# Kernel optimization log

Measured on AMD Instinct MI355X. Metric: run time of the kernel, lower is better.

The kernel has to match this reference:

```python
import jax, jax.numpy as jnp
import numpy as np

B, CQ, CKV, LQ, LKV, HEADS = 4, 1024, 1024, 2048, 2048, 16


def _conv1x1(W, x):
    # Conv1d with kernel size 1: out[b,o,l] = sum_i W[o,i] * x[b,i,l]
    return jnp.einsum('oi,bil->bol', W, x)


def _linear_interp(x, L_out):
    # F.interpolate(mode='linear', align_corners=False) on (B,C,L)
    B_, C_, L_in = x.shape
    if L_in == L_out:
        return x
    scale = L_in / L_out
    pos = (jnp.arange(L_out, dtype=x.dtype) + 0.5) * scale - 0.5
    pos = jnp.clip(pos, 0.0, L_in - 1)
    lo = jnp.floor(pos).astype(jnp.int32)
    hi = jnp.minimum(lo + 1, L_in - 1)
    w = (pos - lo.astype(x.dtype))
    return x[:, :, lo] * (1.0 - w) + x[:, :, hi] * w


def setup_inputs() -> dict:
    key = jax.random.key(0)
    ks = jax.random.split(key, 7)
    winit = 1.0 / np.sqrt(CQ)
    return {
        'query': jax.random.normal(ks[0], (B, CQ, LQ), dtype=jnp.float32),
        'context': jax.random.normal(ks[1], (B, CKV, LKV), dtype=jnp.float32),
        'Wq': jax.random.normal(ks[2], (CQ, CQ), dtype=jnp.float32) * winit,
        'Wk': jax.random.normal(ks[3], (CQ, CKV), dtype=jnp.float32) * winit,
        'Wv': jax.random.normal(ks[4], (CQ, CKV), dtype=jnp.float32) * winit,
        'Wo': jax.random.normal(ks[5], (CQ, CQ), dtype=jnp.float32) * winit,
        'bo': jnp.zeros((CQ,), dtype=jnp.float32),
        'heads': HEADS,
    }


def reference(query, context, Wq, Wk, Wv, Wo, bo, heads):
    B_, Cq, Lq = query.shape
    H = heads
    D = Cq // H
    scale = D ** (-0.5)
    q = _conv1x1(Wq, query).reshape(B_, H, D, Lq)
    k = _conv1x1(Wk, context)
    v = _conv1x1(Wv, context)
    if k.shape[2] != Lq:
        k = _linear_interp(k, Lq)
        v = _linear_interp(v, Lq)
    k = k.reshape(B_, H, D, Lq)
    v = v.reshape(B_, H, D, Lq)
    attn = jnp.einsum('bhdi,bhdj->bhij', q, k) * scale
    attn = jax.nn.softmax(attn, axis=-1)
    out = jnp.einsum('bhij,bhdj->bhdi', attn, v).reshape(B_, Cq, Lq)
    return _conv1x1(Wo, out) + bo[None, :, None] + query
```

## Files before the change

### kernel.cpp

```cpp
#include <hip/hip_runtime.h>
#include <hip/hip_bf16.h>

typedef __bf16 bf16;
typedef __attribute__((ext_vector_type(8))) __bf16 bf16x8;
typedef __attribute__((ext_vector_type(4))) __bf16 bf16x4;
typedef __attribute__((ext_vector_type(4))) float f32x4;
typedef __attribute__((ext_vector_type(8))) float f32x8;
typedef __attribute__((ext_vector_type(16))) float f32x16;
typedef unsigned int uint2v __attribute__((ext_vector_type(2)));

#define B_ 4
#define C_ 1024
#define L_ 2048
#define H_ 16
#define D_ 64

__device__ __forceinline__ int swz(int row, int g) {
    return row * 64 + (((g ^ row) & 7) << 3);
}

__device__ __forceinline__ void async_ld16(const bf16* g, bf16* l) {
    __builtin_amdgcn_global_load_lds(
        (const __attribute__((address_space(1))) unsigned int*)g,
        (__attribute__((address_space(3))) unsigned int*)l, 16, 0, 0);
}

__device__ __forceinline__ float fast_exp2(float x) {
    float r;
    asm("v_exp_f32 %0, %1" : "=v"(r) : "v"(x));
    return r;
}

__global__ void cvt_w4(const float* __restrict__ wq, const float* __restrict__ wk,
                       const float* __restrict__ wv, const float* __restrict__ wo,
                       bf16* __restrict__ oq, bf16* __restrict__ ok,
                       bf16* __restrict__ ov, bf16* __restrict__ oo,
                       float qscale) {
    int z = blockIdx.y;
    const float* in = (z == 0) ? wq : (z == 1) ? wk : (z == 2) ? wv : wo;
    bf16* out       = (z == 0) ? oq : (z == 1) ? ok : (z == 2) ? ov : oo;
    float scale     = (z == 0) ? qscale : 1.0f;
    int i = (blockIdx.x * blockDim.x + threadIdx.x) * 4;
    f32x4 x = *(const f32x4*)&in[i];
    bf16x4 y;
#pragma unroll
    for (int e = 0; e < 4; e++) y[e] = (bf16)(x[e] * scale);
    *(bf16x4*)&out[i] = y;
}

__global__ void transpose_cvt(const float* __restrict__ in, bf16* __restrict__ out) {
    __shared__ bf16 s[32][33];
    int z  = blockIdx.z;
    int c0 = blockIdx.x * 32;
    int r0 = blockIdx.y * 32;
    const float* pin = in + (size_t)z * C_ * L_;
    bf16* pout       = out + (size_t)z * L_ * C_;
#pragma unroll
    for (int k = 0; k < 4; k++) {
        int r = r0 + threadIdx.y + k * 8;
        s[threadIdx.y + k * 8][threadIdx.x] = (bf16)pin[(size_t)r * L_ + c0 + threadIdx.x];
    }
    __syncthreads();
#pragma unroll
    for (int k = 0; k < 4; k++) {
        int c = c0 + threadIdx.y + k * 8;
        pout[(size_t)c * C_ + r0 + threadIdx.x] = s[threadIdx.x][threadIdx.y + k * 8];
    }
}

__global__ __launch_bounds__(256) void gemm_tn(const bf16* __restrict__ A,
                                               const bf16* __restrict__ Wt,
                                               bf16* __restrict__ Dd,
                                               int M, int N, int K) {
    __shared__ __align__(16) bf16 As[2][128 * 64];
    __shared__ __align__(16) bf16 Ws[2][128 * 64];
    int m0 = blockIdx.x * 128, n0 = blockIdx.y * 128;
    int t = threadIdx.x;
    int lane = t & 63, wave = t >> 6;
    int l15 = lane & 15, quad = lane >> 4;
    int wm = (wave >> 1) * 64, wn = (wave & 1) * 64;

    f32x4 acc[4][4];
#pragma unroll
    for (int i = 0; i < 4; i++)
#pragma unroll
        for (int j = 0; j < 4; j++) {
            f32x4 z = {0.f, 0.f, 0.f, 0.f};
            acc[i][j] = z;
        }

    int r8 = lane >> 3;
    int gl = (((lane & 7) ^ r8) & 7) * 8;
    const bf16* aG = A  + (size_t)(m0 + wave * 32 + r8) * K + gl;
    const bf16* wG = Wt + (size_t)(n0 + wave * 32 + r8) * K + gl;

    auto STAGE = [&](int buf, int kk) {
#pragma unroll
        for (int p = 0; p < 4; p++) {
            async_ld16(aG + kk + (size_t)p * 8 * K, &As[buf][(wave * 32 + p * 8) * 64]);
            async_ld16(wG + kk + (size_t)p * 8 * K, &Ws[buf][(wave * 32 + p * 8) * 64]);
        }
    };

    STAGE(0, 0);
    int KT = K >> 6;
    for (int it = 0; it < KT; ++it) {
        int cur = it & 1;
        if (it + 1 < KT) {
            STAGE(cur ^ 1, (it + 1) << 6);
            asm volatile("s_waitcnt vmcnt(8)" ::: "memory");
        } else {
            asm volatile("s_waitcnt vmcnt(0)" ::: "memory");
        }
        __builtin_amdgcn_s_barrier();
        asm volatile("" ::: "memory");
#pragma unroll
        for (int ks = 0; ks < 2; ks++) {
            bf16x8 af[4], bfr[4];
#pragma unroll
            for (int i = 0; i < 4; i++)
                af[i] = *(const bf16x8*)&As[cur][swz(wm + i * 16 + l15, ks * 4 + quad)];
#pragma unroll
            for (int i = 0; i < 4; i++)
                bfr[i] = *(const bf16x8*)&Ws[cur][swz(wn + i * 16 + l15, ks * 4 + quad)];
#pragma unroll
            for (int mt = 0; mt < 4; mt++)
#pragma unroll
                for (int nt = 0; nt < 4; nt++)
                    acc[mt][nt] = __builtin_amdgcn_mfma_f32_16x16x32_bf16(
                        af[mt], bfr[nt], acc[mt][nt], 0, 0, 0);
        }
        asm volatile("" ::: "memory");
        __builtin_amdgcn_s_barrier();
    }
#pragma unroll
    for (int mt = 0; mt < 4; mt++)
#pragma unroll
        for (int nt = 0; nt < 4; nt++)
#pragma unroll
            for (int r = 0; r < 4; r++) {
                int row = m0 + wm + mt * 16 + quad * 4 + r;
                int col = n0 + wn + nt * 16 + l15;
                Dd[(size_t)row * N + col] = (bf16)acc[mt][nt][r];
            }
}

__global__ __launch_bounds__(256) void gemm_v_tn(const bf16* __restrict__ Wv,
                                                 const bf16* __restrict__ ctxT_,
                                                 bf16* __restrict__ vv_) {
    __shared__ __align__(16) bf16 As[2][128 * 64];
    __shared__ __align__(16) bf16 Ws[2][128 * 64];
    int zb = blockIdx.z;
    const bf16* Bz = ctxT_ + (size_t)zb * L_ * C_;
    bf16* vv       = vv_   + (size_t)zb * C_ * L_;

    int m0 = blockIdx.x * 128, n0 = blockIdx.y * 128;
    int t = threadIdx.x;
    int lane = t & 63, wave = t >> 6;
    int l15 = lane & 15, quad = lane >> 4;
    int wm = (wave >> 1) * 64, wn = (wave & 1) * 64;

    f32x4 acc[4][4];
#pragma unroll
    for (int i = 0; i < 4; i++)
#pragma unroll
        for (int j = 0; j < 4; j++) {
            f32x4 z = {0.f, 0.f, 0.f, 0.f};
            acc[i][j] = z;
        }

    int r8 = lane >> 3;
    int gl = (((lane & 7) ^ r8) & 7) * 8;
    const bf16* aG = Wv + (size_t)(m0 + wave * 32 + r8) * C_ + gl;
    const bf16* wG = Bz + (size_t)(n0 + wave * 32 + r8) * C_ + gl;

    auto STAGE = [&](int buf, int kk) {
#pragma unroll
        for (int p = 0; p < 4; p++) {
            async_ld16(aG + kk + (size_t)p * 8 * C_, &As[buf][(wave * 32 + p * 8) * 64]);
            async_ld16(wG + kk + (size_t)p * 8 * C_, &Ws[buf][(wave * 32 + p * 8) * 64]);
        }
    };

    STAGE(0, 0);
    const int KT = C_ >> 6;
    for (int it = 0; it < KT; ++it) {
        int cur = it & 1;
        if (it + 1 < KT) {
            STAGE(cur ^ 1, (it + 1) << 6);
            asm volatile("s_waitcnt vmcnt(8)" ::: "memory");
        } else {
            asm volatile("s_waitcnt vmcnt(0)" ::: "memory");
        }
        __builtin_amdgcn_s_barrier();
        asm volatile("" ::: "memory");
#pragma unroll
        for (int ks = 0; ks < 2; ks++) {
            bf16x8 af[4], bfr[4];
#pragma unroll
            for (int i = 0; i < 4; i++)
                af[i] = *(const bf16x8*)&As[cur][swz(wm + i * 16 + l15, ks * 4 + quad)];
#pragma unroll
            for (int i = 0; i < 4; i++)
                bfr[i] = *(const bf16x8*)&Ws[cur][swz(wn + i * 16 + l15, ks * 4 + quad)];
#pragma unroll
            for (int mt = 0; mt < 4; mt++)
#pragma unroll
                for (int nt = 0; nt < 4; nt++)
                    acc[mt][nt] = __builtin_amdgcn_mfma_f32_16x16x32_bf16(
                        af[mt], bfr[nt], acc[mt][nt], 0, 0, 0);
        }
        asm volatile("" ::: "memory");
        __builtin_amdgcn_s_barrier();
    }
#pragma unroll
    for (int mt = 0; mt < 4; mt++)
#pragma unroll
        for (int nt = 0; nt < 4; nt++)
#pragma unroll
            for (int r = 0; r < 4; r++) {
                int row = m0 + wm + mt * 16 + quad * 4 + r;
                int col = n0 + wn + nt * 16 + l15;
                vv[(size_t)row * L_ + col] = (bf16)acc[mt][nt][r];
            }
}

__global__ __launch_bounds__(256) void gemm_o_final(const bf16* __restrict__ A_,
                                                    const bf16* __restrict__ Wt,
                                                    const float* __restrict__ query_,
                                                    const float* __restrict__ bo,
                                                    float* __restrict__ out_) {
    __shared__ __align__(16) bf16 smem[4 * 128 * 64];

    int zb = blockIdx.z;
    const bf16* A      = A_     + (size_t)zb * L_ * C_;
    const float* query = query_ + (size_t)zb * C_ * L_;
    float* out         = out_   + (size_t)zb * C_ * L_;

    int l0 = blockIdx.x * 128, n0 = blockIdx.y * 128;
    int t = threadIdx.x;
    int lane = t & 63, wave = t >> 6;
    int l15 = lane & 15, quad = lane >> 4;
    int wm = (wave >> 1) * 64, wn = (wave & 1) * 64;

    f32x4 acc[4][4];
#pragma unroll
    for (int i = 0; i < 4; i++)
#pragma unroll
        for (int j = 0; j < 4; j++) {
            f32x4 z = {0.f, 0.f, 0.f, 0.f};
            acc[i][j] = z;
        }

    int r8 = lane >> 3;
    int gl = (((lane & 7) ^ r8) & 7) * 8;
    const bf16* aG = A  + (size_t)(l0 + wave * 32 + r8) * C_ + gl;
    const bf16* wG = Wt + (size_t)(n0 + wave * 32 + r8) * C_ + gl;

    auto STAGE = [&](int buf, int kk) {
        bf16* Ab = smem + buf * 8192;
        bf16* Wb = smem + 16384 + buf * 8192;
#pragma unroll
        for (int p = 0; p < 4; p++) {
            async_ld16(aG + kk + (size_t)p * 8 * C_, &Ab[(wave * 32 + p * 8) * 64]);
            async_ld16(wG + kk + (size_t)p * 8 * C_, &Wb[(wave * 32 + p * 8) * 64]);
        }
    };

    STAGE(0, 0);
    const int KT = C_ >> 6;
    for (int it = 0; it < KT; ++it) {
        int cur = it & 1;
        if (it + 1 < KT) {
            STAGE(cur ^ 1, (it + 1) << 6);
            asm volatile("s_waitcnt vmcnt(8)" ::: "memory");
        } else {
            asm volatile("s_waitcnt vmcnt(0)" ::: "memory");
        }
        __builtin_amdgcn_s_barrier();
        asm volatile("" ::: "memory");
        const bf16* Ab = smem + cur * 8192;
        const bf16* Wb = smem + 16384 + cur * 8192;
#pragma unroll
        for (int ks = 0; ks < 2; ks++) {
            bf16x8 af[4], bfr[4];
#pragma unroll
            for (int i = 0; i < 4; i++)
                af[i] = *(const bf16x8*)&Ab[swz(wm + i * 16 + l15, ks * 4 + quad)];
#pragma unroll
            for (int i = 0; i < 4; i++)
                bfr[i] = *(const bf16x8*)&Wb[swz(wn + i * 16 + l15, ks * 4 + quad)];
#pragma unroll
            for (int mt = 0; mt < 4; mt++)
#pragma unroll
                for (int nt = 0; nt < 4; nt++)
                    acc[mt][nt] = __builtin_amdgcn_mfma_f32_16x16x32_bf16(
                        af[mt], bfr[nt], acc[mt][nt], 0, 0, 0);
        }
        asm volatile("" ::: "memory");
        __builtin_amdgcn_s_barrier();
    }
    __syncthreads();

    bf16 (*Ts)[136] = (bf16 (*)[136])smem;
#pragma unroll
    for (int mt = 0; mt < 4; mt++)
#pragma unroll
        for (int nt = 0; nt < 4; nt++)
#pragma unroll
            for (int r = 0; r < 4; r++)
                Ts[wn + nt * 16 + l15][wm + mt * 16 + quad * 4 + r] = (bf16)acc[mt][nt][r];
    __syncthreads();
#pragma unroll
    for (int j = 0; j < 8; j++) {
        int idx = t + 256 * j;
        int cl  = idx >> 4;
        int ll8 = (idx & 15) * 8;
        int c   = n0 + cl;
        size_t goff = (size_t)c * L_ + l0 + ll8;
        bf16x8 y = *(const bf16x8*)&Ts[cl][ll8];
        f32x8 q = *(const f32x8*)&query[goff];
        float bias = bo[c];
        f32x8 o;
#pragma unroll
        for (int e = 0; e < 8; e++)
            o[e] = (float)y[e] + bias + q[e];
        *(f32x8*)&out[goff] = o;
    }
}

__global__ __launch_bounds__(256) void flash_attn(const bf16* qT,
                                                  const bf16* __restrict__ kT,
                                                  const bf16* __restrict__ v,
                                                  bf16* oT) {
    __shared__ __align__(16) bf16 Ks[2][64 * 64];
    __shared__ __align__(16) bf16 Vs[2][64 * 64];
    int i0 = blockIdx.x * 128;
    int h  = blockIdx.y;
    int zb = blockIdx.z;
    int t = threadIdx.x, lane = t & 63, wave = t >> 6;
    int l31 = lane & 31, kh = lane >> 5;

    const bf16* qB = qT + (size_t)zb * L_ * C_ + (size_t)h * D_;
    const bf16* kB = kT + (size_t)zb * L_ * C_ + (size_t)h * D_;
    const bf16* vB = v  + (size_t)zb * C_ * L_ + (size_t)h * D_ * L_;
    bf16* oB       = oT + (size_t)zb * L_ * C_ + (size_t)h * D_;

    bf16x8 qf[4];
#pragma unroll
    for (int kt = 0; kt < 4; kt++)
        qf[kt] = *(const bf16x8*)&qB[(size_t)(i0 + wave * 32 + l31) * C_ +
                                     kt * 16 + kh * 8];

    f32x16 acc_o[2];
#pragma unroll
    for (int dt = 0; dt < 2; dt++)
#pragma unroll
        for (int r = 0; r < 16; r++) acc_o[dt][r] = 0.f;
    f32x16 acc_l;
#pragma unroll
    for (int r = 0; r < 16; r++) acc_l[r] = 0.f;
    f32x16 z16;
#pragma unroll
    for (int r = 0; r < 16; r++) z16[r] = 0.f;

    bf16x8 onesf;
#pragma unroll
    for (int e = 0; e < 8; e++) onesf[e] = (bf16)1.0f;

    int r8 = lane >> 3;
    int gl = (((lane & 7) ^ r8) & 7) * 8;
    const bf16* kG = kB + (size_t)(wave * 16 + r8) * C_ + gl;
    const bf16* vG = vB + (size_t)(wave * 16 + r8) * L_ + gl;

    auto STAGE = [&](int buf, int j0n) {
#pragma unroll
        for (int p = 0; p < 2; p++) {
            async_ld16(kG + (size_t)j0n * C_ + (size_t)p * 8 * C_,
                       &Ks[buf][(wave * 16 + p * 8) * 64]);
            async_ld16(vG + j0n + (size_t)p * 8 * L_,
                       &Vs[buf][(wave * 16 + p * 8) * 64]);
        }
    };

    STAGE(0, 0);

    const int NT = L_ / 64;
    for (int it = 0; it < NT; ++it) {
        int cur = it & 1;
        if (it + 1 < NT) {
            STAGE(cur ^ 1, (it + 1) * 64);
            asm volatile("s_waitcnt vmcnt(4)" ::: "memory");
        } else {
            asm volatile("s_waitcnt vmcnt(0)" ::: "memory");
        }
        __builtin_amdgcn_s_barrier();
        asm volatile("" ::: "memory");

        const bf16* kb = &Ks[cur][0];
        const bf16* vb = &Vs[cur][0];

#pragma unroll
        for (int jt = 0; jt < 2; jt++) {
            f32x16 s;
            {
                bf16x8 a = *(const bf16x8*)&kb[swz(jt * 32 + l31, kh)];
                s = __builtin_amdgcn_mfma_f32_32x32x16_bf16(a, qf[0], z16, 0, 0, 0);
            }
#pragma unroll
            for (int kt = 1; kt < 4; kt++) {
                bf16x8 a = *(const bf16x8*)&kb[swz(jt * 32 + l31, kt * 2 + kh)];
                s = __builtin_amdgcn_mfma_f32_32x32x16_bf16(a, qf[kt], s, 0, 0, 0);
            }
            unsigned w[4][2];
#pragma unroll
            for (int q = 0; q < 4; q++)
#pragma unroll
                for (int c = 0; c < 2; c++) {
                    float p0 = fast_exp2(s[q * 4 + 2 * c]);
                    float p1 = fast_exp2(s[q * 4 + 2 * c + 1]);
                    asm("v_cvt_pk_bf16_f32 %0, %1, %2"
                        : "=v"(w[q][c]) : "v"(p0), "v"(p1));
                }
#pragma unroll
            for (int kp = 0; kp < 2; kp++) {
                int ks = jt * 2 + kp;
                uint2v r0 = __builtin_amdgcn_permlane32_swap(
                    w[kp * 2][0], w[kp * 2 + 1][0], false, false);
                uint2v r1 = __builtin_amdgcn_permlane32_swap(
                    w[kp * 2][1], w[kp * 2 + 1][1], false, false);
                union { unsigned u[4]; bf16x8 v8; } af;
                af.u[0] = r0[0]; af.u[1] = r1[0];
                af.u[2] = r0[1]; af.u[3] = r1[1];
#pragma unroll
                for (int dt = 0; dt < 2; dt++) {
                    bf16x8 b = *(const bf16x8*)&vb[swz(dt * 32 + l31, ks * 2 + kh)];
                    acc_o[dt] = __builtin_amdgcn_mfma_f32_32x32x16_bf16(
                        af.v8, b, acc_o[dt], 0, 0, 0);
                }
                acc_l = __builtin_amdgcn_mfma_f32_32x32x16_bf16(
                    af.v8, onesf, acc_l, 0, 0, 0);
            }
        }
        asm volatile("" ::: "memory");
        __builtin_amdgcn_s_barrier();
    }

    float inv[16];
#pragma unroll
    for (int r = 0; r < 16; r++) inv[r] = __builtin_amdgcn_rcpf(acc_l[r]);
#pragma unroll
    for (int dt = 0; dt < 2; dt++)
#pragma unroll
        for (int q = 0; q < 4; q++)
#pragma unroll
            for (int r = 0; r < 4; r++) {
                int row = i0 + wave * 32 + 8 * q + 4 * kh + r;
                oB[(size_t)row * C_ + dt * 32 + l31] =
                    (bf16)(acc_o[dt][q * 4 + r] * inv[q * 4 + r]);
            }
}

extern "C" void kernel_launch(void* const* d_in, const int* in_sizes, int n_in,
                              void* d_out, int out_size, void* d_ws, size_t ws_size,
                              hipStream_t stream) {
    const float* query   = (const float*)d_in[0];
    const float* context = (const float*)d_in[1];
    const float* Wq = (const float*)d_in[2];
    const float* Wk = (const float*)d_in[3];
    const float* Wv = (const float*)d_in[4];
    const float* Wo = (const float*)d_in[5];
    const float* bo = (const float*)d_in[6];
    float* out = (float*)d_out;

    const size_t Sw = (size_t)C_ * C_;
    size_t need_batched = (4 * Sw + 3 * (size_t)B_ * L_ * C_) * sizeof(bf16);
    int nb = (ws_size >= need_batched) ? B_ : 1;

    const size_t Sslot = (size_t)nb * L_ * C_;
    bf16* WqB = (bf16*)d_ws;
    bf16* WkB = WqB + Sw;
    bf16* WvB = WkB + Sw;
    bf16* WoB = WvB + Sw;
    bf16* slotA = WoB + Sw;
    bf16* slotB = slotA + Sslot;
    bf16* slotC = slotB + Sslot;

    cvt_w4<<<dim3((unsigned)(Sw / 4 / 256), 4), 256, 0, stream>>>(
        Wq, Wk, Wv, Wo, WqB, WkB, WvB, WoB, 0.1803368801111204f);

    dim3 tb(32, 8);
    dim3 tg(L_ / 32, C_ / 32, nb);
    dim3 gg(nb * L_ / 128, C_ / 128);
    dim3 vg(C_ / 128, L_ / 128, nb);
    dim3 zg(L_ / 128, C_ / 128, nb);
    dim3 fg(L_ / 128, H_, nb);

    for (int b0 = 0; b0 < B_; b0 += nb) {
        const float* qx = query   + (size_t)b0 * C_ * L_;
        const float* cx = context + (size_t)b0 * C_ * L_;
        float* ob       = out     + (size_t)b0 * C_ * L_;

        bf16* vscr = (bf16*)ob;

        transpose_cvt<<<tg, tb, 0, stream>>>(qx, slotA);
        gemm_tn<<<gg, 256, 0, stream>>>(slotA, WqB, slotB, nb * L_, C_, C_);
        transpose_cvt<<<tg, tb, 0, stream>>>(cx, slotA);
        gemm_tn<<<gg, 256, 0, stream>>>(slotA, WkB, slotC, nb * L_, C_, C_);
        gemm_v_tn<<<vg, 256, 0, stream>>>(WvB, slotA, vscr);
        flash_attn<<<fg, 256, 0, stream>>>(slotB, slotC, vscr, slotB);
        gemm_o_final<<<zg, 256, 0, stream>>>(slotB, WoB, qx, bo, ob);
    }
}
```

Measured before the change: 333.9 us.

## Fuse Q/K/V projections and transposes, swizzle block order, triple-buffer attention

Merges the two transpose kernels into one launch and the three projection GEMMs into one grid with a segment index, so fewer launches run and each grid is fuller. GEMM epilogues now stage through LDS for vectorized 16-byte stores. Block indices are remapped across groups of eight in the GEMM and attention grids, apparently to spread neighbouring tiles across XCDs for L2 locality. Flash attention moves to a three-stage K/V pipeline, which uses more LDS and may reduce occupancy. The context transpose is stored in the output buffer as scratch, which relies on that buffer being large enough.

Result: faster. 309.9 us (-7.2%).

```diff
diff --git a/kernel.cpp b/kernel.cpp
--- a/kernel.cpp
+++ b/kernel.cpp
@@ -48,13 +48,18 @@
     *(bf16x4*)&out[i] = y;
 }
 
-__global__ void transpose_cvt(const float* __restrict__ in, bf16* __restrict__ out) {
+__global__ void transpose_cvt2(const float* __restrict__ q,
+                               const float* __restrict__ c,
+                               bf16* __restrict__ qo, bf16* __restrict__ co,
+                               int nb) {
     __shared__ bf16 s[32][33];
     int z  = blockIdx.z;
+    const float* pin;
+    bf16* pout;
+    if (z < nb) { pin = q + (size_t)z * C_ * L_;        pout = qo + (size_t)z * L_ * C_; }
+    else        { pin = c + (size_t)(z - nb) * C_ * L_; pout = co + (size_t)(z - nb) * L_ * C_; }
     int c0 = blockIdx.x * 32;
     int r0 = blockIdx.y * 32;
-    const float* pin = in + (size_t)z * C_ * L_;
-    bf16* pout       = out + (size_t)z * L_ * C_;
 #pragma unroll
     for (int k = 0; k < 4; k++) {
         int r = r0 + threadIdx.y + k * 8;
@@ -63,18 +68,53 @@
     __syncthreads();
 #pragma unroll
     for (int k = 0; k < 4; k++) {
-        int c = c0 + threadIdx.y + k * 8;
-        pout[(size_t)c * C_ + r0 + threadIdx.x] = s[threadIdx.x][threadIdx.y + k * 8];
-    }
-}
-
-__global__ __launch_bounds__(256) void gemm_tn(const bf16* __restrict__ A,
-                                               const bf16* __restrict__ Wt,
-                                               bf16* __restrict__ Dd,
-                                               int M, int N, int K) {
-    __shared__ __align__(16) bf16 As[2][128 * 64];
-    __shared__ __align__(16) bf16 Ws[2][128 * 64];
-    int m0 = blockIdx.x * 128, n0 = blockIdx.y * 128;
+        int cc = c0 + threadIdx.y + k * 8;
+        pout[(size_t)cc * C_ + r0 + threadIdx.x] = s[threadIdx.x][threadIdx.y + k * 8];
+    }
+}
+
+__global__ __launch_bounds__(256) void gemm_fused3(const bf16* __restrict__ qT,
+                                                   const bf16* __restrict__ ctxT,
+                                                   const bf16* __restrict__ Wq,
+                                                   const bf16* __restrict__ Wk,
+                                                   const bf16* __restrict__ Wv,
+                                                   bf16* __restrict__ qP,
+                                                   bf16* __restrict__ kP,
+                                                   bf16* __restrict__ vP,
+                                                   int nb) {
+    __shared__ __align__(16) bf16 smem[4 * 128 * 64];
+
+    int seg = blockIdx.y;
+    int r   = blockIdx.x;
+    int cpx = nb << 4;
+    int lg  = (r & 7) * cpx + (r >> 3);
+
+    const bf16 *aP, *bP;
+    bf16* dP;
+    int S;
+    if (seg == 0) {
+        int m_idx = lg >> 3, n_idx = lg & 7;
+        aP = qT + (size_t)m_idx * 128 * C_;
+        bP = Wq + (size_t)n_idx * 128 * C_;
+        dP = qP + (size_t)m_idx * 128 * C_ + n_idx * 128;
+        S = C_;
+    } else if (seg == 1) {
+        int m_idx = lg >> 3, n_idx = lg & 7;
+        aP = ctxT + (size_t)m_idx * 128 * C_;
+        bP = Wk + (size_t)n_idx * 128 * C_;
+        dP = kP + (size_t)m_idx * 128 * C_ + n_idx * 128;
+        S = C_;
+    } else {
+        int m_idx = lg & 7;
+        int nt    = lg >> 3;
+        int zb    = nt >> 4;
+        int nc0   = (nt & 15) * 128;
+        aP = Wv + (size_t)m_idx * 128 * C_;
+        bP = ctxT + (size_t)nt * 128 * C_;
+        dP = vP + (size_t)zb * C_ * L_ + (size_t)m_idx * 128 * L_ + nc0;
+        S = L_;
+    }
+
     int t = threadIdx.x;
     int lane = t & 63, wave = t >> 6;
     int l15 = lane & 15, quad = lane >> 4;
@@ -91,94 +131,16 @@
 
     int r8 = lane >> 3;
     int gl = (((lane & 7) ^ r8) & 7) * 8;
-    const bf16* aG = A  + (size_t)(m0 + wave * 32 + r8) * K + gl;
-    const bf16* wG = Wt + (size_t)(n0 + wave * 32 + r8) * K + gl;
+    const bf16* aG = aP + (size_t)(wave * 32 + r8) * C_ + gl;
+    const bf16* wG = bP + (size_t)(wave * 32 + r8) * C_ + gl;
 
     auto STAGE = [&](int buf, int kk) {
+        bf16* Ab = smem + buf * 8192;
+        bf16* Wb = smem + 16384 + buf * 8192;
 #pragma unroll
         for (int p = 0; p < 4; p++) {
-            async_ld16(aG + kk + (size_t)p * 8 * K, &As[buf][(wave * 32 + p * 8) * 64]);
-            async_ld16(wG + kk + (size_t)p * 8 * K, &Ws[buf][(wave * 32 + p * 8) * 64]);
-        }
-    };
-
-    STAGE(0, 0);
-    int KT = K >> 6;
-    for (int it = 0; it < KT; ++it) {
-        int cur = it & 1;
-        if (it + 1 < KT) {
-            STAGE(cur ^ 1, (it + 1) << 6);
-            asm volatile("s_waitcnt vmcnt(8)" ::: "memory");
-        } else {
-            asm volatile("s_waitcnt vmcnt(0)" ::: "memory");
-        }
-        __builtin_amdgcn_s_barrier();
-        asm volatile("" ::: "memory");
-#pragma unroll
-        for (int ks = 0; ks < 2; ks++) {
-            bf16x8 af[4], bfr[4];
-#pragma unroll
-            for (int i = 0; i < 4; i++)
-                af[i] = *(const bf16x8*)&As[cur][swz(wm + i * 16 + l15, ks * 4 + quad)];
-#pragma unroll
-            for (int i = 0; i < 4; i++)
-                bfr[i] = *(const bf16x8*)&Ws[cur][swz(wn + i * 16 + l15, ks * 4 + quad)];
-#pragma unroll
-            for (int mt = 0; mt < 4; mt++)
-#pragma unroll
-                for (int nt = 0; nt < 4; nt++)
-                    acc[mt][nt] = __builtin_amdgcn_mfma_f32_16x16x32_bf16(
-                        af[mt], bfr[nt], acc[mt][nt], 0, 0, 0);
-        }
-        asm volatile("" ::: "memory");
-        __builtin_amdgcn_s_barrier();
-    }
-#pragma unroll
-    for (int mt = 0; mt < 4; mt++)
-#pragma unroll
-        for (int nt = 0; nt < 4; nt++)
-#pragma unroll
-            for (int r = 0; r < 4; r++) {
-                int row = m0 + wm + mt * 16 + quad * 4 + r;
-                int col = n0 + wn + nt * 16 + l15;
-                Dd[(size_t)row * N + col] = (bf16)acc[mt][nt][r];
-            }
-}
-
-__global__ __launch_bounds__(256) void gemm_v_tn(const bf16* __restrict__ Wv,
-                                                 const bf16* __restrict__ ctxT_,
-                                                 bf16* __restrict__ vv_) {
-    __shared__ __align__(16) bf16 As[2][128 * 64];
-    __shared__ __align__(16) bf16 Ws[2][128 * 64];
-    int zb = blockIdx.z;
-    const bf16* Bz = ctxT_ + (size_t)zb * L_ * C_;
-    bf16* vv       = vv_   + (size_t)zb * C_ * L_;
-
-    int m0 = blockIdx.x * 128, n0 = blockIdx.y * 128;
-    int t = threadIdx.x;
-    int lane = t & 63, wave = t >> 6;
-    int l15 = lane & 15, quad = lane >> 4;
-    int wm = (wave >> 1) * 64, wn = (wave & 1) * 64;
-
-    f32x4 acc[4][4];
-#pragma unroll
-    for (int i = 0; i < 4; i++)
-#pragma unroll
-        for (int j = 0; j < 4; j++) {
-            f32x4 z = {0.f, 0.f, 0.f, 0.f};
-            acc[i][j] = z;
-        }
-
-    int r8 = lane >> 3;
-    int gl = (((lane & 7) ^ r8) & 7) * 8;
-    const bf16* aG = Wv + (size_t)(m0 + wave * 32 + r8) * C_ + gl;
-    const bf16* wG = Bz + (size_t)(n0 + wave * 32 + r8) * C_ + gl;
-
-    auto STAGE = [&](int buf, int kk) {
-#pragma unroll
-        for (int p = 0; p < 4; p++) {
-            async_ld16(aG + kk + (size_t)p * 8 * C_, &As[buf][(wave * 32 + p * 8) * 64]);
-            async_ld16(wG + kk + (size_t)p * 8 * C_, &Ws[buf][(wave * 32 + p * 8) * 64]);
+            async_ld16(aG + kk + (size_t)p * 8 * C_, &Ab[(wave * 32 + p * 8) * 64]);
+            async_ld16(wG + kk + (size_t)p * 8 * C_, &Wb[(wave * 32 + p * 8) * 64]);
         }
     };
 
@@ -194,50 +156,69 @@
         }
         __builtin_amdgcn_s_barrier();
         asm volatile("" ::: "memory");
+        const bf16* Ab = smem + cur * 8192;
+        const bf16* Wb = smem + 16384 + cur * 8192;
 #pragma unroll
         for (int ks = 0; ks < 2; ks++) {
             bf16x8 af[4], bfr[4];
 #pragma unroll
             for (int i = 0; i < 4; i++)
-                af[i] = *(const bf16x8*)&As[cur][swz(wm + i * 16 + l15, ks * 4 + quad)];
+                af[i] = *(const bf16x8*)&Ab[swz(wm + i * 16 + l15, ks * 4 + quad)];
 #pragma unroll
             for (int i = 0; i < 4; i++)
-                bfr[i] = *(const bf16x8*)&Ws[cur][swz(wn + i * 16 + l15, ks * 4 + quad)];
+                bfr[i] = *(const bf16x8*)&Wb[swz(wn + i * 16 + l15, ks * 4 + quad)];
 #pragma unroll
             for (int mt = 0; mt < 4; mt++)
 #pragma unroll
-                for (int nt = 0; nt < 4; nt++)
-                    acc[mt][nt] = __builtin_amdgcn_mfma_f32_16x16x32_bf16(
-                        af[mt], bfr[nt], acc[mt][nt], 0, 0, 0);
-        }
-        asm volatile("" ::: "memory");
-        __builtin_amdgcn_s_barrier();
-    }
+                for (int nt2 = 0; nt2 < 4; nt2++)
+                    acc[mt][nt2] = __builtin_amdgcn_mfma_f32_16x16x32_bf16(
+                        af[mt], bfr[nt2], acc[mt][nt2], 0, 0, 0);
+        }
+        asm volatile("" ::: "memory");
+        __builtin_amdgcn_s_barrier();
+    }
+    __syncthreads();
+
+    bf16 (*Ts2)[136] = (bf16 (*)[136])smem;
 #pragma unroll
     for (int mt = 0; mt < 4; mt++)
 #pragma unroll
-        for (int nt = 0; nt < 4; nt++)
-#pragma unroll
-            for (int r = 0; r < 4; r++) {
-                int row = m0 + wm + mt * 16 + quad * 4 + r;
-                int col = n0 + wn + nt * 16 + l15;
-                vv[(size_t)row * L_ + col] = (bf16)acc[mt][nt][r];
-            }
+        for (int nt2 = 0; nt2 < 4; nt2++)
+#pragma unroll
+            for (int rr = 0; rr < 4; rr++)
+                Ts2[wm + mt * 16 + quad * 4 + rr][wn + nt2 * 16 + l15] =
+                    (bf16)acc[mt][nt2][rr];
+    __syncthreads();
+#pragma unroll
+    for (int j = 0; j < 8; j++) {
+        int idx = t + 256 * j;
+        int ml  = idx >> 4;
+        int nl8 = (idx & 15) * 8;
+        bf16x8 x = *(const bf16x8*)&Ts2[ml][nl8];
+        *(bf16x8*)&dP[(size_t)ml * S + nl8] = x;
+    }
 }
 
 __global__ __launch_bounds__(256) void gemm_o_final(const bf16* __restrict__ A_,
                                                     const bf16* __restrict__ Wt,
                                                     const float* __restrict__ query_,
                                                     const float* __restrict__ bo,
-                                                    float* __restrict__ out_) {
+                                                    float* __restrict__ out_,
+                                                    int nb) {
     __shared__ __align__(16) bf16 smem[4 * 128 * 64];
 
-    int zb = blockIdx.z;
-    const bf16* A      = A_     + (size_t)zb * L_ * C_;
+    int bid = blockIdx.x;
+    int cpx = nb << 4;
+    int lg  = (bid & 7) * cpx + (bid >> 3);
+    int m   = lg >> 3;
+    int n0  = (lg & 7) * 128;
+    int zb  = m >> 4;
+    int l0  = (m & 15) * 128;
+
+    const bf16* A      = A_ + (size_t)m * 128 * C_;
     const float* query = query_ + (size_t)zb * C_ * L_;
     float* out         = out_   + (size_t)zb * C_ * L_;
 
-    int l0 = blockIdx.x * 128, n0 = blockIdx.y * 128;
     int t = threadIdx.x;
     int lane = t & 63, wave = t >> 6;
     int l15 = lane & 15, quad = lane >> 4;
@@ -254,7 +235,7 @@
 
     int r8 = lane >> 3;
     int gl = (((lane & 7) ^ r8) & 7) * 8;
-    const bf16* aG = A  + (size_t)(l0 + wave * 32 + r8) * C_ + gl;
+    const bf16* aG = A  + (size_t)(wave * 32 + r8) * C_ + gl;
     const bf16* wG = Wt + (size_t)(n0 + wave * 32 + r8) * C_ + gl;
 
     auto STAGE = [&](int buf, int kk) {
@@ -308,8 +289,8 @@
 #pragma unroll
         for (int nt = 0; nt < 4; nt++)
 #pragma unroll
-            for (int r = 0; r < 4; r++)
-                Ts[wn + nt * 16 + l15][wm + mt * 16 + quad * 4 + r] = (bf16)acc[mt][nt][r];
+            for (int rr = 0; rr < 4; rr++)
+                Ts[wn + nt * 16 + l15][wm + mt * 16 + quad * 4 + rr] = (bf16)acc[mt][nt][rr];
     __syncthreads();
 #pragma unroll
     for (int j = 0; j < 8; j++) {
@@ -333,11 +314,15 @@
                                                   const bf16* __restrict__ kT,
                                                   const bf16* __restrict__ v,
                                                   bf16* oT) {
-    __shared__ __align__(16) bf16 Ks[2][64 * 64];
-    __shared__ __align__(16) bf16 Vs[2][64 * 64];
-    int i0 = blockIdx.x * 128;
-    int h  = blockIdx.y;
-    int zb = blockIdx.z;
+    __shared__ __align__(16) bf16 Ks[3][64 * 64];
+    __shared__ __align__(16) bf16 Vs[3][64 * 64];
+    int bid = blockIdx.x;
+    int cpx = gridDim.x >> 3;
+    int logical = (bid & 7) * cpx + (bid >> 3);
+    int i0 = (logical & 15) * 128;
+    int g  = logical >> 4;
+    int h  = g & 15;
+    int zb = g >> 4;
     int t = threadIdx.x, lane = t & 63, wave = t >> 6;
     int l31 = lane & 31, kh = lane >> 5;
 
@@ -384,12 +369,15 @@
     };
 
     STAGE(0, 0);
+    STAGE(1, 64);
 
     const int NT = L_ / 64;
+    int cur = 0, sb = 2;
     for (int it = 0; it < NT; ++it) {
-        int cur = it & 1;
-        if (it + 1 < NT) {
-            STAGE(cur ^ 1, (it + 1) * 64);
+        if (it + 2 < NT) {
+            STAGE(sb, (it + 2) * 64);
+            asm volatile("s_waitcnt vmcnt(8)" ::: "memory");
+        } else if (it + 1 < NT) {
             asm volatile("s_waitcnt vmcnt(4)" ::: "memory");
         } else {
             asm volatile("s_waitcnt vmcnt(0)" ::: "memory");
@@ -444,6 +432,8 @@
         }
         asm volatile("" ::: "memory");
         __builtin_amdgcn_s_barrier();
+        cur = (cur == 2) ? 0 : cur + 1;
+        sb  = (sb  == 2) ? 0 : sb  + 1;
     }
 
     float inv[16];
@@ -490,25 +480,20 @@
         Wq, Wk, Wv, Wo, WqB, WkB, WvB, WoB, 0.1803368801111204f);
 
     dim3 tb(32, 8);
-    dim3 tg(L_ / 32, C_ / 32, nb);
-    dim3 gg(nb * L_ / 128, C_ / 128);
-    dim3 vg(C_ / 128, L_ / 128, nb);
-    dim3 zg(L_ / 128, C_ / 128, nb);
-    dim3 fg(L_ / 128, H_, nb);
 
     for (int b0 = 0; b0 < B_; b0 += nb) {
         const float* qx = query   + (size_t)b0 * C_ * L_;
         const float* cx = context + (size_t)b0 * C_ * L_;
         float* ob       = out     + (size_t)b0 * C_ * L_;
 
-        bf16* vscr = (bf16*)ob;
-
-        transpose_cvt<<<tg, tb, 0, stream>>>(qx, slotA);
-        gemm_tn<<<gg, 256, 0, stream>>>(slotA, WqB, slotB, nb * L_, C_, C_);
-        transpose_cvt<<<tg, tb, 0, stream>>>(cx, slotA);
-        gemm_tn<<<gg, 256, 0, stream>>>(slotA, WkB, slotC, nb * L_, C_, C_);
-        gemm_v_tn<<<vg, 256, 0, stream>>>(WvB, slotA, vscr);
-        flash_attn<<<fg, 256, 0, stream>>>(slotB, slotC, vscr, slotB);
-        gemm_o_final<<<zg, 256, 0, stream>>>(slotB, WoB, qx, bo, ob);
-    }
-}
+        bf16* vscr  = (bf16*)ob;
+        bf16* ctxTs = (bf16*)ob + Sslot;
+
+        transpose_cvt2<<<dim3(L_ / 32, C_ / 32, 2 * nb), tb, 0, stream>>>(
+            qx, cx, slotA, ctxTs, nb);
+        gemm_fused3<<<dim3(128 * nb, 3), 256, 0, stream>>>(
+            slotA, ctxTs, WqB, WkB, WvB, slotB, slotC, vscr, nb);
+        flash_attn<<<256 * nb, 256, 0, stream>>>(slotB, slotC, vscr, slotB);
+        gemm_o_final<<<128 * nb, 256, 0, stream>>>(slotB, WoB, qx, bo, ob, nb);
+    }
+}
```
